# Kernel tuning notes

Hardware: AMD Instinct MI355X
Metric: run time of the kernel (lower is better)

Reference implementation:

```python
import jax, jax.numpy as jnp
import numpy as np

N, C, H, E = 4096, 512, 8, 131072
D = C // H
ALPHA = 0.5
EPS = 1e-5


def layer_norm(x, g, b):
    mu = jnp.mean(x, axis=-1, keepdims=True)
    var = jnp.mean((x - mu) ** 2, axis=-1, keepdims=True)
    return (x - mu) * jax.lax.rsqrt(var + EPS) * g + b


def setup_inputs() -> dict:
    key = jax.random.key(0)
    ks = jax.random.split(key, 20)
    s = 0.02
    return {
        "x": jax.random.normal(ks[0], (N, C), jnp.float32),
        "edge_index": jax.random.randint(ks[1], (2, E), 0, N, jnp.int32),
        "local_w": jax.random.normal(ks[2], (C, C), jnp.float32) * s,
        "local_b": jnp.zeros((C,), jnp.float32),
        "in_proj_w": jax.random.normal(ks[3], (3 * C, C), jnp.float32) * s,
        "in_proj_b": jnp.zeros((3 * C,), jnp.float32),
        "attn_out_w": jax.random.normal(ks[4], (C, C), jnp.float32) * s,
        "attn_out_b": jnp.zeros((C,), jnp.float32),
        "output_w": jax.random.normal(ks[5], (C, C), jnp.float32) * s,
        "output_b": jnp.zeros((C,), jnp.float32),
        "norm1_g": jnp.ones((C,), jnp.float32),
        "norm1_b": jnp.zeros((C,), jnp.float32),
        "norm2_g": jnp.ones((C,), jnp.float32),
        "norm2_b": jnp.zeros((C,), jnp.float32),
        "ffn_w1": jax.random.normal(ks[6], (2 * C, C), jnp.float32) * s,
        "ffn_b1": jnp.zeros((2 * C,), jnp.float32),
        "ffn_w2": jax.random.normal(ks[7], (C, 2 * C), jnp.float32) * s,
        "ffn_b2": jnp.zeros((C,), jnp.float32),
    }


def reference(x, edge_index, local_w, local_b, in_proj_w, in_proj_b,
              attn_out_w, attn_out_b, output_w, output_b,
              norm1_g, norm1_b, norm2_g, norm2_b,
              ffn_w1, ffn_b1, ffn_w2, ffn_b2):
    src, dst = edge_index[0], edge_index[1]

    # local branch: linear then scatter-mean over incoming edges
    local_h = x @ local_w.T + local_b                       # [N,C]
    summed = jax.ops.segment_sum(local_h[src], dst, num_segments=N)
    cnt = jax.ops.segment_sum(jnp.ones((E,), x.dtype), dst, num_segments=N)
    local_out = summed / jnp.maximum(cnt, 1.0)[:, None]

    # global branch: full self-attention over all nodes
    qkv = x @ in_proj_w.T + in_proj_b                       # [N,3C]
    q, k, v = jnp.split(qkv, 3, axis=-1)
    q = q.reshape(N, H, D)
    k = k.reshape(N, H, D)
    v = v.reshape(N, H, D)
    scores = jnp.einsum('nhd,mhd->hnm', q, k) / jnp.sqrt(jnp.asarray(D, x.dtype))
    attn = jax.nn.softmax(scores, axis=-1)                  # [H,N,N]
    ctx = jnp.einsum('hnm,mhd->nhd', attn, v).reshape(N, C)
    global_out = ctx @ attn_out_w.T + attn_out_b

    mixed = ALPHA * local_out + (1.0 - ALPHA) * global_out
    hidden = layer_norm(x + (mixed @ output_w.T + output_b), norm1_g, norm1_b)

    ff = jax.nn.gelu(hidden @ ffn_w1.T + ffn_b1, approximate=False) @ ffn_w2.T + ffn_b2
    return layer_norm(hidden + ff, norm2_g, norm2_b)
```

## Files before the change

### kernel.cpp

```cpp
#include <hip/hip_runtime.h>


#define N_NODES 4096
#define C_DIM   512
#define H_HEADS 8
#define D_HEAD  64
#define E_EDGES 131072

typedef unsigned short u16;
typedef unsigned int   u32;
typedef u16   u16x8  __attribute__((ext_vector_type(8)));
typedef __bf16 bf16x8 __attribute__((ext_vector_type(8)));
typedef float  f32x4  __attribute__((ext_vector_type(4)));
typedef u32    u32x4  __attribute__((ext_vector_type(4)));

__device__ __forceinline__ float b2f(u16 u) {
  unsigned int i = ((unsigned int)u) << 16;
  return __builtin_bit_cast(float, i);
}
__device__ __forceinline__ u16 f2b(float f) {
  unsigned int i = __builtin_bit_cast(unsigned int, f);
  i += 0x7fffu + ((i >> 16) & 1u);
  return (u16)(i >> 16);
}
__device__ __forceinline__ u32 cvtpk(float lo, float hi) {
  u32 r;
  asm("v_cvt_pk_bf16_f32 %0, %1, %2" : "=v"(r) : "v"(lo), "v"(hi));
  return r;
}
__device__ __forceinline__ void pl32swap(u32& x, u32& y) {
  asm("v_permlane32_swap_b32 %0, %1" : "+v"(x), "+v"(y));
}
__device__ __forceinline__ void pl16swap(u32& x, u32& y) {
  asm("v_permlane16_swap_b32 %0, %1" : "+v"(x), "+v"(y));
}
__device__ __forceinline__ void glds16(const u16* g, u16* l) {
  __builtin_amdgcn_global_load_lds(
      (const __attribute__((address_space(1))) void*)g,
      (__attribute__((address_space(3))) void*)l, 16, 0, 0);
}

struct CvtArgs {
  const float* src[7];
  u16* dst[7];
  int n[7];
  int* deg;
};

__global__ __launch_bounds__(256) void cvt_multi(CvtArgs a) {
  const int t = blockIdx.y;
  if (t == 7) {
    const int i = blockIdx.x * 256 + threadIdx.x;
    if (i < N_NODES) a.deg[i] = 0;
    return;
  }
  const int i = (blockIdx.x * 256 + threadIdx.x) * 8;
  if (i >= a.n[t]) return;
  const float* s = a.src[t] + i;
  f32x4 v0 = *(const f32x4*)s;
  f32x4 v1 = *(const f32x4*)(s + 4);
  u16x8 o;
  o[0]=f2b(v0[0]); o[1]=f2b(v0[1]); o[2]=f2b(v0[2]); o[3]=f2b(v0[3]);
  o[4]=f2b(v1[0]); o[5]=f2b(v1[1]); o[6]=f2b(v1[2]); o[7]=f2b(v1[3]);
  *(u16x8*)(a.dst[t] + i) = o;
}

template<int EPI>
__global__ __launch_bounds__(256) void gemm_bt(
    const u16* __restrict__ A, const u16* __restrict__ W,
    const float* __restrict__ bias, void* __restrict__ outp,
    int M, int Nout, int K,
    const float* __restrict__ mloc)
{
  const int tid  = threadIdx.x;
  const int lane = tid & 63, wave = tid >> 6;
  const int quad = lane >> 4, l16 = lane & 15;
  const int wm = wave >> 1, wn = wave & 1;
  const int bm = blockIdx.x, bnb = blockIdx.y;

  __shared__ __align__(16) u16 As[64][128];
  __shared__ __align__(16) u16 Ws[64][128];

  f32x4 acc[2][2] = {};

  const int lr4 = lane >> 4, gs = lane & 15;
  const int g8e = (gs ^ lr4) * 8;
  const int g8o = (gs ^ (4 + lr4)) * 8;
  const u16* aw[8];
#pragma unroll
  for (int c = 0; c < 4; ++c) {
    const int g8 = (c & 1) ? g8o : g8e;
    aw[c]     = A + (size_t)(bm  * 64 + wave * 16 + c * 4 + lr4) * K + g8;
    aw[4 + c] = W + (size_t)(bnb * 64 + wave * 16 + c * 4 + lr4) * K + g8;
  }

  for (int k0 = 0; k0 < K; k0 += 128) {
    __syncthreads();
#pragma unroll
    for (int c = 0; c < 4; ++c) {
      glds16(aw[c] + k0,     &As[wave * 16 + c * 4][0]);
      glds16(aw[4 + c] + k0, &Ws[wave * 16 + c * 4][0]);
    }
    __syncthreads();
#pragma unroll
    for (int ks = 0; ks < 4; ++ks) {
      const int slot = ((ks * 4 + quad) ^ (l16 & 7)) * 8;
      bf16x8 af[2], bf[2];
      af[0] = *(const bf16x8*)&As[wm * 32 +      l16][slot];
      af[1] = *(const bf16x8*)&As[wm * 32 + 16 + l16][slot];
      bf[0] = *(const bf16x8*)&Ws[wn * 32 +      l16][slot];
      bf[1] = *(const bf16x8*)&Ws[wn * 32 + 16 + l16][slot];
#pragma unroll
      for (int i = 0; i < 2; ++i)
#pragma unroll
        for (int j = 0; j < 2; ++j)
          acc[i][j] = __builtin_amdgcn_mfma_f32_16x16x32_bf16(af[i], bf[j], acc[i][j], 0, 0, 0);
    }
  }

#pragma unroll
  for (int i = 0; i < 2; ++i)
#pragma unroll
    for (int j = 0; j < 2; ++j) {
      const int col = bnb * 64 + wn * 32 + j * 16 + l16;
      const float bias_v = bias[col];
#pragma unroll
      for (int r = 0; r < 4; ++r) {
        const int row = bm * 64 + wm * 32 + i * 16 + quad * 4 + r;
        float v = acc[i][j][r] + bias_v;
        const size_t o = (size_t)row * Nout + col;
        if constexpr (EPI == 1) {
          ((float*)outp)[o] = v;
        } else if constexpr (EPI == 2) {
          float gl = 0.5f * v * (1.0f + erff(v * 0.70710678118654752f));
          ((u16*)outp)[o] = f2b(gl);
        } else {
          ((u16*)outp)[o] = f2b(0.5f * mloc[o] + 0.5f * v);
        }
      }
    }
}

__global__ __launch_bounds__(256) void gemm128(
    const u16* __restrict__ A, const u16* __restrict__ W,
    const float* __restrict__ bias0, const float* __restrict__ bias1,
    u16* __restrict__ out0, u16* __restrict__ out1,
    int M, int Nout, int K,
    const int* __restrict__ ei, int* __restrict__ deg)
{
  const int tid  = threadIdx.x;
  if (blockIdx.y == 16) {
#pragma unroll
    for (int i = 0; i < 16; ++i) {
      const int e = blockIdx.x * 4096 + i * 256 + tid;
      atomicAdd(&deg[ei[E_EDGES + e]], 1);
    }
    return;
  }
  const int lane = tid & 63, wave = tid >> 6;
  const int quad = lane >> 4, l16 = lane & 15;
  const int wm = wave >> 1, wn = wave & 1;
  const int bm = blockIdx.x, bnb = blockIdx.y;

  __shared__ __align__(16) u16 As[128][64];
  __shared__ __align__(16) u16 Ws[128][64];

  f32x4 acc[4][4] = {};

  const int lr = lane >> 3, gs = lane & 7;
  const int g8 = (gs ^ lr) * 8;
  const u16* ab = A + (size_t)(bm  * 128 + wave * 32 + lr) * K + g8;
  const u16* wb = W + (size_t)(bnb * 128 + wave * 32 + lr) * K + g8;

  for (int k0 = 0; k0 < K; k0 += 64) {
    __syncthreads();
#pragma unroll
    for (int c = 0; c < 4; ++c) {
      glds16(ab + (size_t)(c * 8) * K + k0, &As[wave * 32 + c * 8][0]);
      glds16(wb + (size_t)(c * 8) * K + k0, &Ws[wave * 32 + c * 8][0]);
    }
    __syncthreads();
#pragma unroll
    for (int ks = 0; ks < 2; ++ks) {
      const int slot = ((ks * 4 + quad) ^ (l16 & 7)) * 8;
      bf16x8 af[4], bf[4];
#pragma unroll
      for (int am = 0; am < 4; ++am)
        af[am] = *(const bf16x8*)&As[wm * 64 + am * 16 + l16][slot];
#pragma unroll
      for (int bn = 0; bn < 4; ++bn)
        bf[bn] = *(const bf16x8*)&Ws[wn * 64 + bn * 16 + l16][slot];
#pragma unroll
      for (int am = 0; am < 4; ++am)
#pragma unroll
        for (int bn = 0; bn < 4; ++bn)
          acc[am][bn] = __builtin_amdgcn_mfma_f32_16x16x32_bf16(af[am], bf[bn], acc[am][bn], 0, 0, 0);
    }
  }

#pragma unroll
  for (int am = 0; am < 4; ++am)
#pragma unroll
    for (int bn = 0; bn < 4; ++bn) {
      const int col = bnb * 128 + wn * 64 + bn * 16 + l16;
      const float bias_v = (col < 512) ? bias0[col] : bias1[col - 512];
#pragma unroll
      for (int r = 0; r < 4; ++r) {
        const int row = bm * 128 + wm * 64 + am * 16 + quad * 4 + r;
        float v = acc[am][bn][r] + bias_v;
        if (col < 512) out0[(size_t)row * 512 + col] = f2b(v);
        else           out1[(size_t)row * 1536 + (col - 512)] = f2b(v);
      }
    }
}

__global__ __launch_bounds__(256) void scan_vtrans(
    const int* __restrict__ deg, int* __restrict__ off, int* __restrict__ cursor,
    const u16* __restrict__ qkv, u16* __restrict__ vt)
{
  if (blockIdx.x == 512) {
    __shared__ int part[256];
    const int t = threadIdx.x;
    int v[16];
    int s = 0;
#pragma unroll
    for (int i = 0; i < 16; ++i) { v[i] = deg[t * 16 + i]; s += v[i]; }
    part[t] = s;
    __syncthreads();
    for (int d = 1; d < 256; d <<= 1) {
      int val = (t >= d) ? part[t - d] : 0;
      __syncthreads();
      if (t >= d) part[t] += val;
      __syncthreads();
    }
    int prefix = (t == 0) ? 0 : part[t - 1];
#pragma unroll
    for (int i = 0; i < 16; ++i) {
      off[t * 16 + i] = prefix;
      cursor[t * 16 + i] = prefix;
      prefix += v[i];
    }
    if (t == 255) off[4096] = prefix;
    return;
  }
  __shared__ __align__(16) u16 T[64][64];
  const int tid = threadIdx.x;
  const int h = blockIdx.x >> 6, mt = blockIdx.x & 63;
  const int m0 = mt * 64;
  const int c  = tid & 7;
  const int mr = tid >> 3;
#pragma unroll
  for (int half = 0; half < 2; ++half) {
    const int m = mr + half * 32;
    const u16x8 v = *(const u16x8*)(qkv + (size_t)(m0 + m) * 1536 + 1024 + h * 64 + c * 8);
    *(u16x8*)&T[m][((c ^ (m >> 3)) * 8)] = v;
  }
  __syncthreads();
#pragma unroll
  for (int half = 0; half < 2; ++half) {
    const int q = tid + half * 256;
    const int d = q >> 3, mc = q & 7;
    u16x8 w;
#pragma unroll
    for (int e = 0; e < 8; ++e)
      w[e] = T[mc * 8 + e][(((d >> 3) ^ mc) * 8) + (d & 7)];
    *(u16x8*)(vt + (size_t)(h * 64 + d) * N_NODES + m0 + mc * 8) = w;
  }
}

template<int SPLITS>
__global__ __launch_bounds__(256) void attn_kernel(
    const u16* __restrict__ qkv, const u16* __restrict__ vt,
    u16* __restrict__ opart, float* __restrict__ lpart,
    const int* __restrict__ ei, int* __restrict__ cursor, int* __restrict__ csr)
{
  const int tid = threadIdx.x, wave = tid >> 6, lane = tid & 63;
  const int split = blockIdx.z;
  if (split == SPLITS) {
    const int sblk = blockIdx.y * 32 + blockIdx.x;
#pragma unroll
    for (int i = 0; i < 2; ++i) {
      const int e = sblk * 512 + i * 256 + tid;
      const int s = ei[e];
      const int d = ei[E_EDGES + e];
      const int p = atomicAdd(&cursor[d], 1);
      csr[p] = s;
    }
    return;
  }
  const int quad = lane >> 4, l16 = lane & 15;
  const int h = blockIdx.y, tile = blockIdx.x;

  __shared__ __align__(16) u16 Ks[2][64][64];
  __shared__ __align__(16) u16 Vts[3][64][64];

  const float QSCALE = 0.18033688011112042f;
  bf16x8 aq[2][2];
#pragma unroll
  for (int mb = 0; mb < 2; ++mb) {
    const int qrow = tile * 128 + wave * 32 + mb * 16 + l16;
    const u16* qp = qkv + (size_t)qrow * 1536 + h * 64 + quad * 8;
    u16x8 q0 = *(const u16x8*)qp;
    u16x8 q1 = *(const u16x8*)(qp + 32);
    u16x8 s0, s1;
#pragma unroll
    for (int i = 0; i < 8; ++i) {
      s0[i] = f2b(b2f(q0[i]) * QSCALE);
      s1[i] = f2b(b2f(q1[i]) * QSCALE);
    }
    aq[mb][0] = __builtin_bit_cast(bf16x8, s0);
    aq[mb][1] = __builtin_bit_cast(bf16x8, s1);
  }

  f32x4 O[2][4] = {};
  float lsum[2] = {};

  const int lr = lane >> 3, gs = lane & 7;
  const int g8 = (gs ^ lr) * 8;
  const int R0 = wave * 16 + lr;

  const u16* kp = qkv + (size_t)R0 * 1536 + 512 + h * 64 + g8;
  const u16* vp = vt + (size_t)(h * 64 + R0) * N_NODES + g8;

  const int mt0 = split * (64 / SPLITS), mt1 = (split + 1) * (64 / SPLITS);

  {
    const size_t ko = (size_t)mt0 * 64 * 1536;
    glds16(kp + ko,            &Ks[0][wave * 16][0]);
    glds16(kp + ko + 8 * 1536, &Ks[0][wave * 16 + 8][0]);
    glds16(vp + mt0 * 64,               &Vts[0][wave * 16][0]);
    glds16(vp + mt0 * 64 + 8 * N_NODES, &Vts[0][wave * 16 + 8][0]);
  }

  bf16x8 paP[2][2];
  int vprev = 2, vcur = 0, vnext = 1;

  for (int mt = mt0; mt < mt1; ++mt) {
    const int kc = (mt - mt0) & 1;
    if (mt + 1 < mt1) {
      const size_t ko = (size_t)(mt + 1) * 64 * 1536;
      glds16(kp + ko,            &Ks[kc ^ 1][wave * 16][0]);
      glds16(kp + ko + 8 * 1536, &Ks[kc ^ 1][wave * 16 + 8][0]);
      glds16(vp + (mt + 1) * 64,               &Vts[vnext][wave * 16][0]);
      glds16(vp + (mt + 1) * 64 + 8 * N_NODES, &Vts[vnext][wave * 16 + 8][0]);
      asm volatile("s_waitcnt vmcnt(4)" ::: "memory");
    } else {
      asm volatile("s_waitcnt vmcnt(0)" ::: "memory");
    }
    __builtin_amdgcn_s_barrier();
    __builtin_amdgcn_sched_barrier(0);

    __builtin_amdgcn_s_setprio(1);
    f32x4 st[2][4] = {};
#pragma unroll
    for (int ks = 0; ks < 2; ++ks) {
      const int slot = ((ks * 4 + quad) ^ (l16 & 7)) * 8;
      bf16x8 af[4];
#pragma unroll
      for (int jn = 0; jn < 4; ++jn)
        af[jn] = *(const bf16x8*)&Ks[kc][jn * 16 + l16][slot];
#pragma unroll
      for (int mb = 0; mb < 2; ++mb)
#pragma unroll
        for (int jn = 0; jn < 4; ++jn)
          st[mb][jn] = __builtin_amdgcn_mfma_f32_16x16x32_bf16(af[jn], aq[mb][ks], st[mb][jn], 0, 0, 0);
    }
    if (mt > mt0) {
#pragma unroll
      for (int ks = 0; ks < 2; ++ks) {
        const int slot = ((ks * 4 + quad) ^ (l16 & 7)) * 8;
        bf16x8 bv[4];
#pragma unroll
        for (int jd = 0; jd < 4; ++jd)
          bv[jd] = *(const bf16x8*)&Vts[vprev][jd * 16 + l16][slot];
#pragma unroll
        for (int mb = 0; mb < 2; ++mb)
#pragma unroll
          for (int jd = 0; jd < 4; ++jd)
            O[mb][jd] = __builtin_amdgcn_mfma_f32_16x16x32_bf16(paP[mb][ks], bv[jd], O[mb][jd], 0, 0, 0);
      }
    }
    __builtin_amdgcn_s_setprio(0);

#pragma unroll
    for (int mb = 0; mb < 2; ++mb) {
      u32 pk[4][2];
#pragma unroll
      for (int jn = 0; jn < 4; ++jn) {
        float p0 = __builtin_amdgcn_exp2f(st[mb][jn][0]);
        float p1 = __builtin_amdgcn_exp2f(st[mb][jn][1]);
        float p2 = __builtin_amdgcn_exp2f(st[mb][jn][2]);
        float p3 = __builtin_amdgcn_exp2f(st[mb][jn][3]);
        lsum[mb] += (p0 + p1) + (p2 + p3);
        pk[jn][0] = cvtpk(p0, p1);
        pk[jn][1] = cvtpk(p2, p3);
      }
#pragma unroll
      for (int ks = 0; ks < 2; ++ks) {
        u32 x0 = pk[2 * ks][0], y0 = pk[2 * ks + 1][0];
        u32 x1 = pk[2 * ks][1], y1 = pk[2 * ks + 1][1];
        pl32swap(x0, y0); pl16swap(x0, y0);
        pl32swap(x1, y1); pl16swap(x1, y1);
        u32x4 av;
        av[0] = x0; av[1] = x1; av[2] = y0; av[3] = y1;
        paP[mb][ks] = __builtin_bit_cast(bf16x8, av);
      }
    }

    __builtin_amdgcn_s_barrier();
    const int vr = vprev; vprev = vcur; vcur = vnext; vnext = vr;
  }

#pragma unroll
  for (int ks = 0; ks < 2; ++ks) {
    const int slot = ((ks * 4 + quad) ^ (l16 & 7)) * 8;
    bf16x8 bv[4];
#pragma unroll
    for (int jd = 0; jd < 4; ++jd)
      bv[jd] = *(const bf16x8*)&Vts[vprev][jd * 16 + l16][slot];
#pragma unroll
    for (int mb = 0; mb < 2; ++mb)
#pragma unroll
      for (int jd = 0; jd < 4; ++jd)
        O[mb][jd] = __builtin_amdgcn_mfma_f32_16x16x32_bf16(paP[mb][ks], bv[jd], O[mb][jd], 0, 0, 0);
  }

#pragma unroll
  for (int mb = 0; mb < 2; ++mb) {
    float ls = lsum[mb];
    ls += __shfl_xor(ls, 16);
    ls += __shfl_xor(ls, 32);
#pragma unroll
    for (int r = 0; r < 4; ++r) {
      const int row = tile * 128 + wave * 32 + mb * 16 + quad * 4 + r;
      u16* orow = opart + ((size_t)split * N_NODES + row) * C_DIM + h * 64;
#pragma unroll
      for (int jd = 0; jd < 4; ++jd)
        orow[jd * 16 + l16] = f2b(O[mb][jd][r]);
    }
    if (lane < 16) {
      const int row = tile * 128 + wave * 32 + mb * 16 + l16;
      lpart[((size_t)split * N_NODES + row) * H_HEADS + h] = ls;
    }
  }
}

template<int SPLITS>
__global__ __launch_bounds__(256) void combine_gather(
    const u16* __restrict__ opart, const float* __restrict__ lpart,
    u16* __restrict__ ctx,
    const int* __restrict__ off, const int* __restrict__ csr,
    const u16* __restrict__ lh, float* __restrict__ lo)
{
  if (blockIdx.y == 0) {
    const int wave = threadIdx.x >> 6, lane = threadIdx.x & 63;
    const int n = blockIdx.x * 4 + wave;
    const int j0 = off[n], j1 = off[n + 1];
    float acc[8] = {};
    int j = j0;
    for (; j + 4 <= j1; j += 4) {
      const int s0 = csr[j], s1 = csr[j + 1], s2 = csr[j + 2], s3 = csr[j + 3];
      const u16x8 v0 = *(const u16x8*)(lh + (size_t)s0 * C_DIM + lane * 8);
      const u16x8 v1 = *(const u16x8*)(lh + (size_t)s1 * C_DIM + lane * 8);
      const u16x8 v2 = *(const u16x8*)(lh + (size_t)s2 * C_DIM + lane * 8);
      const u16x8 v3 = *(const u16x8*)(lh + (size_t)s3 * C_DIM + lane * 8);
#pragma unroll
      for (int i = 0; i < 8; ++i)
        acc[i] += (b2f(v0[i]) + b2f(v1[i])) + (b2f(v2[i]) + b2f(v3[i]));
    }
    for (; j < j1; ++j) {
      const int s = csr[j];
      const u16x8 v = *(const u16x8*)(lh + (size_t)s * C_DIM + lane * 8);
#pragma unroll
      for (int i = 0; i < 8; ++i) acc[i] += b2f(v[i]);
    }
    const float inv = 1.0f / fmaxf((float)(j1 - j0), 1.0f);
    f32x4 o0, o1;
#pragma unroll
    for (int i = 0; i < 4; ++i) { o0[i] = acc[i] * inv; o1[i] = acc[4 + i] * inv; }
    float* op = lo + (size_t)n * C_DIM + lane * 8;
    *(f32x4*)op = o0;
    *(f32x4*)(op + 4) = o1;
    return;
  }
  const size_t base = (size_t)(blockIdx.x * 256 + threadIdx.x) * 8;
  const int row = (int)(base >> 9);
  const int h = (int)((base & 511) >> 6);
  float l = 0.0f;
#pragma unroll
  for (int s = 0; s < SPLITS; ++s)
    l += lpart[(size_t)s * N_NODES * H_HEADS + (size_t)row * H_HEADS + h];
  const float inv = 1.0f / l;
  float o[8] = {};
#pragma unroll
  for (int s = 0; s < SPLITS; ++s) {
    const u16x8 p = *(const u16x8*)(opart + (size_t)s * N_NODES * C_DIM + base);
#pragma unroll
    for (int i = 0; i < 8; ++i) o[i] += b2f(p[i]);
  }
  u16x8 ob;
#pragma unroll
  for (int i = 0; i < 8; ++i) ob[i] = f2b(o[i] * inv);
  *(u16x8*)(ctx + base) = ob;
}

__global__ __launch_bounds__(256) void ln1_kernel(
    const float* __restrict__ x, const float* __restrict__ pr,
    const float* __restrict__ g, const float* __restrict__ b,
    u16* __restrict__ hb, float* __restrict__ hf)
{
  const int wave = threadIdx.x >> 6, lane = threadIdx.x & 63;
  const int row = blockIdx.x * 4 + wave;
  const int c0 = lane * 8;
  const size_t base = (size_t)row * C_DIM + c0;
  f32x4 x0 = *(const f32x4*)(x + base);
  f32x4 x1 = *(const f32x4*)(x + base + 4);
  f32x4 p0 = *(const f32x4*)(pr + base);
  f32x4 p1 = *(const f32x4*)(pr + base + 4);
  float v[8];
#pragma unroll
  for (int i = 0; i < 4; ++i) { v[i] = x0[i] + p0[i]; v[4 + i] = x1[i] + p1[i]; }
  float sum = 0, sq = 0;
#pragma unroll
  for (int i = 0; i < 8; ++i) { sum += v[i]; sq += v[i] * v[i]; }
  for (int off = 1; off < 64; off <<= 1) { sum += __shfl_xor(sum, off); sq += __shfl_xor(sq, off); }
  const float mean = sum * (1.0f / C_DIM);
  const float var  = sq * (1.0f / C_DIM) - mean * mean;
  const float rstd = rsqrtf(var + 1e-5f);
  f32x4 g0 = *(const f32x4*)(g + c0), g1 = *(const f32x4*)(g + c0 + 4);
  f32x4 b0 = *(const f32x4*)(b + c0), b1 = *(const f32x4*)(b + c0 + 4);
  u16x8 ob; f32x4 h0, h1;
#pragma unroll
  for (int i = 0; i < 4; ++i) {
    float hv0 = (v[i]     - mean) * rstd * g0[i] + b0[i];
    float hv1 = (v[4 + i] - mean) * rstd * g1[i] + b1[i];
    h0[i] = hv0; h1[i] = hv1;
    ob[i] = f2b(hv0); ob[4 + i] = f2b(hv1);
  }
  *(u16x8*)(hb + base) = ob;
  *(f32x4*)(hf + base) = h0;
  *(f32x4*)(hf + base + 4) = h1;
}

__global__ __launch_bounds__(256) void ln2_kernel(
    const float* __restrict__ a, const float* __restrict__ c,
    const float* __restrict__ g, const float* __restrict__ b,
    float* __restrict__ out)
{
  const int wave = threadIdx.x >> 6, lane = threadIdx.x & 63;
  const int row = blockIdx.x * 4 + wave;
  const int c0 = lane * 8;
  const size_t base = (size_t)row * C_DIM + c0;
  f32x4 a0 = *(const f32x4*)(a + base), a1 = *(const f32x4*)(a + base + 4);
  f32x4 c0v = *(const f32x4*)(c + base), c1v = *(const f32x4*)(c + base + 4);
  float v[8];
#pragma unroll
  for (int i = 0; i < 4; ++i) { v[i] = a0[i] + c0v[i]; v[4 + i] = a1[i] + c1v[i]; }
  float sum = 0, sq = 0;
#pragma unroll
  for (int i = 0; i < 8; ++i) { sum += v[i]; sq += v[i] * v[i]; }
  for (int off = 1; off < 64; off <<= 1) { sum += __shfl_xor(sum, off); sq += __shfl_xor(sq, off); }
  const float mean = sum * (1.0f / C_DIM);
  const float var  = sq * (1.0f / C_DIM) - mean * mean;
  const float rstd = rsqrtf(var + 1e-5f);
  f32x4 g0 = *(const f32x4*)(g + c0), g1 = *(const f32x4*)(g + c0 + 4);
  f32x4 b0 = *(const f32x4*)(b + c0), b1 = *(const f32x4*)(b + c0 + 4);
  f32x4 h0, h1;
#pragma unroll
  for (int i = 0; i < 4; ++i) {
    h0[i] = (v[i]     - mean) * rstd * g0[i] + b0[i];
    h1[i] = (v[4 + i] - mean) * rstd * g1[i] + b1[i];
  }
  *(f32x4*)(out + base) = h0;
  *(f32x4*)(out + base + 4) = h1;
}

extern "C" void kernel_launch(void* const* d_in, const int* in_sizes, int n_in,
                              void* d_out, int out_size, void* d_ws, size_t ws_size,
                              hipStream_t stream) {
  const float* x          = (const float*)d_in[0];
  const int*   ei         = (const int*)d_in[1];
  const float* local_w    = (const float*)d_in[2];
  const float* local_b    = (const float*)d_in[3];
  const float* in_proj_w  = (const float*)d_in[4];
  const float* in_proj_b  = (const float*)d_in[5];
  const float* attn_out_w = (const float*)d_in[6];
  const float* attn_out_b = (const float*)d_in[7];
  const float* output_w   = (const float*)d_in[8];
  const float* output_b   = (const float*)d_in[9];
  const float* n1g = (const float*)d_in[10];
  const float* n1b = (const float*)d_in[11];
  const float* n2g = (const float*)d_in[12];
  const float* n2b = (const float*)d_in[13];
  const float* ffn_w1 = (const float*)d_in[14];
  const float* ffn_b1 = (const float*)d_in[15];
  const float* ffn_w2 = (const float*)d_in[16];
  const float* ffn_b2 = (const float*)d_in[17];
  float* out = (float*)d_out;

  char* ws = (char*)d_ws;
  size_t o = 0;
  float* local_out = (float*)(ws + o); o += (size_t)N_NODES * C_DIM * 4;
  int* deg    = (int*)(ws + o); o += (N_NODES) * 4;
  int* off    = (int*)(ws + o); o += (N_NODES + 16) * 4;
  int* cursor = (int*)(ws + o); o += (N_NODES) * 4;
  int* csr    = (int*)(ws + o); o += (size_t)E_EDGES * 4;
  u16* xb   = (u16*)(ws + o); o += (size_t)N_NODES * C_DIM * 2;
  u16* wbLQ = (u16*)(ws + o); o += (size_t)4 * C_DIM * C_DIM * 2;
  u16* wbA  = (u16*)(ws + o); o += (size_t)C_DIM * C_DIM * 2;
  u16* wbO  = (u16*)(ws + o); o += (size_t)C_DIM * C_DIM * 2;
  u16* wbF1 = (u16*)(ws + o); o += (size_t)2 * C_DIM * C_DIM * 2;
  u16* wbF2 = (u16*)(ws + o); o += (size_t)2 * C_DIM * C_DIM * 2;
  u16* local_h   = (u16*)(ws + o); o += (size_t)N_NODES * C_DIM * 2;
  u16* qkvb      = (u16*)(ws + o); o += (size_t)N_NODES * 3 * C_DIM * 2;
  u16* ctxb      = (u16*)(ws + o); o += (size_t)N_NODES * C_DIM * 2;
  u16* mixed     = (u16*)(ws + o); o += (size_t)N_NODES * C_DIM * 2;
  u16* hidden_bf = (u16*)(ws + o); o += (size_t)N_NODES * C_DIM * 2;
  float* hidden_f = (float*)(ws + o); o += (size_t)N_NODES * C_DIM * 4;
  u16* ff1       = (u16*)(ws + o); o += (size_t)N_NODES * 2 * C_DIM * 2;
  float* proj  = (float*)qkvb;
  float* ff2   = (float*)local_out;
  u16*   vt    = xb;
  u16* opart4 = (u16*)(ws + o);
  float* lpart4 = (float*)(ws + o + (size_t)4 * N_NODES * C_DIM * 2);
  const size_t need4 = o + (size_t)4 * N_NODES * C_DIM * 2 + (size_t)4 * N_NODES * H_HEADS * 4;
  const bool use4 = (ws_size >= need4);
  u16* opart2 = (u16*)hidden_bf;
  float* lpart2 = (float*)(opart2 + (size_t)2 * N_NODES * C_DIM);

  CvtArgs ca;
  ca.src[0] = x;          ca.dst[0] = xb;   ca.n[0] = N_NODES * C_DIM;
  ca.src[1] = local_w;    ca.dst[1] = wbLQ;                  ca.n[1] = C_DIM * C_DIM;
  ca.src[2] = in_proj_w;  ca.dst[2] = wbLQ + C_DIM * C_DIM;  ca.n[2] = 3 * C_DIM * C_DIM;
  ca.src[3] = attn_out_w; ca.dst[3] = wbA;  ca.n[3] = C_DIM * C_DIM;
  ca.src[4] = output_w;   ca.dst[4] = wbO;  ca.n[4] = C_DIM * C_DIM;
  ca.src[5] = ffn_w1;     ca.dst[5] = wbF1; ca.n[5] = 2 * C_DIM * C_DIM;
  ca.src[6] = ffn_w2;     ca.dst[6] = wbF2; ca.n[6] = 2 * C_DIM * C_DIM;
  ca.deg = deg;
  cvt_multi<<<dim3(N_NODES * C_DIM / 2048, 8), 256, 0, stream>>>(ca);

  gemm128<<<dim3(32, 17), 256, 0, stream>>>(xb, wbLQ, local_b, in_proj_b,
      local_h, qkvb, N_NODES, 4 * C_DIM, C_DIM, ei, deg);

  scan_vtrans<<<513, 256, 0, stream>>>(deg, off, cursor, qkvb, vt);

  if (use4) {
    attn_kernel<4><<<dim3(32, 8, 5), 256, 0, stream>>>(qkvb, vt, opart4, lpart4,
        ei, cursor, csr);
    combine_gather<4><<<dim3(1024, 2), 256, 0, stream>>>(opart4, lpart4, ctxb,
        off, csr, local_h, local_out);
  } else {
    attn_kernel<2><<<dim3(32, 8, 3), 256, 0, stream>>>(qkvb, vt, opart2, lpart2,
        ei, cursor, csr);
    combine_gather<2><<<dim3(1024, 2), 256, 0, stream>>>(opart2, lpart2, ctxb,
        off, csr, local_h, local_out);
  }

  gemm_bt<3><<<dim3(64, 8), 256, 0, stream>>>(ctxb, wbA, attn_out_b, mixed,
      N_NODES, C_DIM, C_DIM, local_out);

  gemm_bt<1><<<dim3(64, 8), 256, 0, stream>>>(mixed, wbO, output_b, proj,
      N_NODES, C_DIM, C_DIM, nullptr);
  ln1_kernel<<<N_NODES / 4, 256, 0, stream>>>(x, proj, n1g, n1b, hidden_bf, hidden_f);

  gemm_bt<2><<<dim3(64, 16), 256, 0, stream>>>(hidden_bf, wbF1, ffn_b1, ff1,
      N_NODES, 2 * C_DIM, C_DIM, nullptr);
  gemm_bt<1><<<dim3(64, 8), 256, 0, stream>>>(ff1, wbF2, ffn_b2, ff2,
      N_NODES, C_DIM, 2 * C_DIM, nullptr);
  ln2_kernel<<<N_NODES / 4, 256, 0, stream>>>(hidden_f, ff2, n2g, n2b, out);
}
```

Measured before the change: 252.1 us.

## Drop software-pipelined PV across iterations and remap grid for head-major block order

Removes the skewed pipeline in which the previous tile's P·V MFMAs ran alongside the current tile's QK^T. The loop now computes S, the softmax probabilities and P·V for the same tile, which lets V use a double buffer instead of a triple buffer and cuts LDS use. Block indices are also remapped so the 8 heads of a query tile are adjacent in blockIdx.x, intended to improve cache sharing of Q rows. The cost is lost overlap between the exp/convert work and the MFMA work within a wave, and the host launch grid dimensions must match the new mapping.

```diff
diff --git a/kernel.cpp b/kernel.cpp
--- a/kernel.cpp
+++ b/kernel.cpp
@@ -289,10 +289,11 @@
     return;
   }
   const int quad = lane >> 4, l16 = lane & 15;
-  const int h = blockIdx.y, tile = blockIdx.x;
+  const int h = blockIdx.x & 7;
+  const int tile = (blockIdx.x >> 3) + (blockIdx.y << 2);
 
   __shared__ __align__(16) u16 Ks[2][64][64];
-  __shared__ __align__(16) u16 Vts[3][64][64];
+  __shared__ __align__(16) u16 Vts[2][64][64];
 
   const float QSCALE = 0.18033688011112042f;
   bf16x8 aq[2][2];
@@ -332,17 +333,14 @@
     glds16(vp + mt0 * 64 + 8 * N_NODES, &Vts[0][wave * 16 + 8][0]);
   }
 
-  bf16x8 paP[2][2];
-  int vprev = 2, vcur = 0, vnext = 1;
-
   for (int mt = mt0; mt < mt1; ++mt) {
-    const int kc = (mt - mt0) & 1;
+    const int cur = (mt - mt0) & 1;
     if (mt + 1 < mt1) {
       const size_t ko = (size_t)(mt + 1) * 64 * 1536;
-      glds16(kp + ko,            &Ks[kc ^ 1][wave * 16][0]);
-      glds16(kp + ko + 8 * 1536, &Ks[kc ^ 1][wave * 16 + 8][0]);
-      glds16(vp + (mt + 1) * 64,               &Vts[vnext][wave * 16][0]);
-      glds16(vp + (mt + 1) * 64 + 8 * N_NODES, &Vts[vnext][wave * 16 + 8][0]);
+      glds16(kp + ko,            &Ks[cur ^ 1][wave * 16][0]);
+      glds16(kp + ko + 8 * 1536, &Ks[cur ^ 1][wave * 16 + 8][0]);
+      glds16(vp + (mt + 1) * 64,               &Vts[cur ^ 1][wave * 16][0]);
+      glds16(vp + (mt + 1) * 64 + 8 * N_NODES, &Vts[cur ^ 1][wave * 16 + 8][0]);
       asm volatile("s_waitcnt vmcnt(4)" ::: "memory");
     } else {
       asm volatile("s_waitcnt vmcnt(0)" ::: "memory");
@@ -350,38 +348,24 @@
     __builtin_amdgcn_s_barrier();
     __builtin_amdgcn_sched_barrier(0);
 
+    f32x4 st[2][4] = {};
     __builtin_amdgcn_s_setprio(1);
-    f32x4 st[2][4] = {};
 #pragma unroll
     for (int ks = 0; ks < 2; ++ks) {
       const int slot = ((ks * 4 + quad) ^ (l16 & 7)) * 8;
       bf16x8 af[4];
 #pragma unroll
       for (int jn = 0; jn < 4; ++jn)
-        af[jn] = *(const bf16x8*)&Ks[kc][jn * 16 + l16][slot];
+        af[jn] = *(const bf16x8*)&Ks[cur][jn * 16 + l16][slot];
 #pragma unroll
       for (int mb = 0; mb < 2; ++mb)
 #pragma unroll
         for (int jn = 0; jn < 4; ++jn)
           st[mb][jn] = __builtin_amdgcn_mfma_f32_16x16x32_bf16(af[jn], aq[mb][ks], st[mb][jn], 0, 0, 0);
     }
-    if (mt > mt0) {
-#pragma unroll
-      for (int ks = 0; ks < 2; ++ks) {
-        const int slot = ((ks * 4 + quad) ^ (l16 & 7)) * 8;
-        bf16x8 bv[4];
-#pragma unroll
-        for (int jd = 0; jd < 4; ++jd)
-          bv[jd] = *(const bf16x8*)&Vts[vprev][jd * 16 + l16][slot];
-#pragma unroll
-        for (int mb = 0; mb < 2; ++mb)
-#pragma unroll
-          for (int jd = 0; jd < 4; ++jd)
-            O[mb][jd] = __builtin_amdgcn_mfma_f32_16x16x32_bf16(paP[mb][ks], bv[jd], O[mb][jd], 0, 0, 0);
-      }
-    }
     __builtin_amdgcn_s_setprio(0);
 
+    bf16x8 pa[2][2];
 #pragma unroll
     for (int mb = 0; mb < 2; ++mb) {
       u32 pk[4][2];
@@ -403,26 +387,26 @@
         pl32swap(x1, y1); pl16swap(x1, y1);
         u32x4 av;
         av[0] = x0; av[1] = x1; av[2] = y0; av[3] = y1;
-        paP[mb][ks] = __builtin_bit_cast(bf16x8, av);
+        pa[mb][ks] = __builtin_bit_cast(bf16x8, av);
       }
     }
 
+    __builtin_amdgcn_s_setprio(1);
+#pragma unroll
+    for (int ks = 0; ks < 2; ++ks) {
+      const int slot = ((ks * 4 + quad) ^ (l16 & 7)) * 8;
+      bf16x8 bv[4];
+#pragma unroll
+      for (int jd = 0; jd < 4; ++jd)
+        bv[jd] = *(const bf16x8*)&Vts[cur][jd * 16 + l16][slot];
+#pragma unroll
+      for (int mb = 0; mb < 2; ++mb)
+#pragma unroll
+        for (int jd = 0; jd < 4; ++jd)
+          O[mb][jd] = __builtin_amdgcn_mfma_f32_16x16x32_bf16(pa[mb][ks], bv[jd], O[mb][jd], 0, 0, 0);
+    }
+    __builtin_amdgcn_s_setprio(0);
     __builtin_amdgcn_s_barrier();
-    const int vr = vprev; vprev = vcur; vcur = vnext; vnext = vr;
-  }
-
-#pragma unroll
-  for (int ks = 0; ks < 2; ++ks) {
-    const int slot = ((ks * 4 + quad) ^ (l16 & 7)) * 8;
-    bf16x8 bv[4];
-#pragma unroll
-    for (int jd = 0; jd < 4; ++jd)
-      bv[jd] = *(const bf16x8*)&Vts[vprev][jd * 16 + l16][slot];
-#pragma unroll
-    for (int mb = 0; mb < 2; ++mb)
-#pragma unroll
-      for (int jd = 0; jd < 4; ++jd)
-        O[mb][jd] = __builtin_amdgcn_mfma_f32_16x16x32_bf16(paP[mb][ks], bv[jd], O[mb][jd], 0, 0, 0);
   }
 
 #pragma unroll
```

New measurement: 242.8 us. 3.7% less time.
